# Kernel tuning notes

Hardware: AMD Instinct MI355X
Metric: run time of the kernel (lower is better)

The kernel has to match this reference:

```python
import jax, jax.numpy as jnp
import numpy as np
import math

B, S, D, H, FF = 4, 2048, 1024, 16, 4096
DH = D // H
EPS = 1e-6


def setup_inputs() -> dict:
    key = jax.random.key(0)
    ks = jax.random.split(key, 12)
    s = 0.02
    inp = {
        "x": jax.random.normal(ks[0], (B, S, D), dtype=jnp.float32),
        "mask": jax.random.randint(ks[1], (B, 1, S, S), 0, 2, dtype=jnp.int32),
        # torch Linear y = x @ W.T + b; we store W already transposed as [in, out]
        "Wq": jax.random.normal(ks[2], (D, D), dtype=jnp.float32) * s,
        "bq": jnp.zeros((D,), jnp.float32),
        "Wk": jax.random.normal(ks[3], (D, D), dtype=jnp.float32) * s,
        "bk": jnp.zeros((D,), jnp.float32),
        "Wv": jax.random.normal(ks[4], (D, D), dtype=jnp.float32) * s,
        "bv": jnp.zeros((D,), jnp.float32),
        "Wo": jax.random.normal(ks[5], (D, D), dtype=jnp.float32) * s,
        "bo": jnp.zeros((D,), jnp.float32),
        "ln1_g": jnp.ones((D,), jnp.float32),
        "ln1_b": jnp.zeros((D,), jnp.float32),
        "W1": jax.random.normal(ks[6], (D, FF), dtype=jnp.float32) * s,
        "b1": jnp.zeros((FF,), jnp.float32),
        "W2": jax.random.normal(ks[7], (FF, D), dtype=jnp.float32) * s,
        "b2": jnp.zeros((D,), jnp.float32),
        "ln2_g": jnp.ones((D,), jnp.float32),
        "ln2_b": jnp.zeros((D,), jnp.float32),
    }
    return inp


def _layer_norm(x, g, b):
    m = jnp.mean(x, axis=-1, keepdims=True)
    v = jnp.mean(jnp.square(x - m), axis=-1, keepdims=True)
    return (x - m) * jax.lax.rsqrt(v + EPS) * g + b


def reference(x, mask, Wq, bq, Wk, bk, Wv, bv, Wo, bo,
              ln1_g, ln1_b, W1, b1, W2, b2, ln2_g, ln2_b):
    # ---- multi-head self-attention (dropout = identity, eval mode) ----
    def split_heads(t):  # [B,S,D] -> [B,H,S,DH]
        return t.reshape(B, S, H, DH).transpose(0, 2, 1, 3)

    q = split_heads(x @ Wq + bq)
    k = split_heads(x @ Wk + bk)
    v = split_heads(x @ Wv + bv)

    scores = jnp.einsum("bhqd,bhkd->bhqk", q, k) / math.sqrt(DH)
    scores = jnp.where(mask == 0, jnp.float32(-1e9), scores)
    attn = jax.nn.softmax(scores, axis=-1)
    out = jnp.einsum("bhqk,bhkd->bhqd", attn, v)
    out = out.transpose(0, 2, 1, 3).reshape(B, S, D)
    attn_out = out @ Wo + bo

    # ---- sublayer 1: x + LayerNorm(attn_out)  (post-applied LN, faithful) ----
    x = x + _layer_norm(attn_out, ln1_g, ln1_b)

    # ---- FFN with exact GELU ----
    ff = jax.nn.gelu(x @ W1 + b1, approximate=False) @ W2 + b2

    # ---- sublayer 2 ----
    x = x + _layer_norm(ff, ln2_g, ln2_b)
    return x
```

## Files before the change

kernel.cpp:

```cpp
#include <hip/hip_runtime.h>
#include <hip/hip_bf16.h>

#define BDIM 4
#define SDIM 2048
#define DDIM 1024
#define HDIM 16
#define FFDIM 4096
#define MROWS (BDIM*SDIM)

using bf16 = __hip_bfloat16;
typedef __attribute__((ext_vector_type(8))) short short8;
typedef __attribute__((ext_vector_type(4))) short short4v;
typedef __attribute__((ext_vector_type(4))) float f32x4;

__device__ __forceinline__ f32x4 mfma16(short8 a, short8 b, f32x4 c) {
  return __builtin_amdgcn_mfma_f32_16x16x32_bf16(a, b, c, 0, 0, 0);
}

__device__ __forceinline__ void gll16(const void* g, void* l) {
  __builtin_amdgcn_global_load_lds((const __attribute__((address_space(1))) void*)g,
                                   (__attribute__((address_space(3))) void*)l, 16, 0, 0);
}

template<int EPI>
__global__ __launch_bounds__(256)
void gemm_bt(const bf16* __restrict__ A, const bf16* __restrict__ Bt,
             const float* __restrict__ bias0, const float* __restrict__ bias1,
             const float* __restrict__ bias2,
             void* __restrict__ Cout, int K, int N)
{
  __shared__ bf16 As[128*32];
  __shared__ bf16 Bs[128*32];
  const int tid  = threadIdx.x;
  const int wave = tid >> 6;
  const int lane = tid & 63;
  const int llo  = lane & 15, lhi = lane >> 4;
  const int row0 = blockIdx.y * 128;
  const int col0 = blockIdx.x * 128;
  const int wm = wave >> 1, wn = wave & 1;

  f32x4 acc[4][4];
#pragma unroll
  for (int i = 0; i < 4; i++)
#pragma unroll
    for (int j = 0; j < 4; j++) acc[i][j] = (f32x4){0.f, 0.f, 0.f, 0.f};

  const int c0 = wave * 2, c1 = wave * 2 + 1;
  const size_t arow0 = (size_t)(row0 + c0*16 + (lane >> 2)) * K;
  const size_t arow1 = (size_t)(row0 + c1*16 + (lane >> 2)) * K;
  const size_t brow0 = (size_t)(col0 + c0*16 + (lane >> 2)) * K;
  const size_t brow1 = (size_t)(col0 + c1*16 + (lane >> 2)) * K;
  const int colb = ((lane & 3) ^ ((lane >> 3) & 3)) * 8;

  const int nkt = K >> 5;
  for (int kt = 0; kt < nkt; ++kt) {
    __syncthreads();
    const int kofs = kt * 32 + colb;
    gll16(A  + arow0 + kofs, As + c0*512);
    gll16(A  + arow1 + kofs, As + c1*512);
    gll16(Bt + brow0 + kofs, Bs + c0*512);
    gll16(Bt + brow1 + kofs, Bs + c1*512);
    __syncthreads();
    short8 af[4], bfr[4];
    const int rsw = (lhi ^ ((llo >> 1) & 3)) * 8;
#pragma unroll
    for (int mi = 0; mi < 4; mi++)
      af[mi] = *(const short8*)(As + (wm*64 + mi*16 + llo)*32 + rsw);
#pragma unroll
    for (int ni = 0; ni < 4; ni++)
      bfr[ni] = *(const short8*)(Bs + (wn*64 + ni*16 + llo)*32 + rsw);
#pragma unroll
    for (int mi = 0; mi < 4; mi++)
#pragma unroll
      for (int ni = 0; ni < 4; ni++)
        acc[mi][ni] = mfma16(af[mi], bfr[ni], acc[mi][ni]);
  }

#pragma unroll
  for (int mi = 0; mi < 4; mi++) {
#pragma unroll
    for (int ni = 0; ni < 4; ni++) {
      const int col = col0 + wn*64 + ni*16 + llo;
      float bv;
      if (EPI == 1) {
        const int which = col >> 10, win = col & 1023;
        const float* bp = (which == 0) ? bias0 : ((which == 1) ? bias1 : bias2);
        bv = bp[win];
      } else {
        bv = bias0[col];
      }
      if (EPI == 1) {
        const int which = col >> 10, win = col & 1023;
        const int h = win >> 6, dh = win & 63;
        if (which < 2) {
#pragma unroll
          for (int r = 0; r < 4; r++) {
            const int row = row0 + wm*64 + mi*16 + lhi*4 + r;
            const int b = row >> 11, s = row & 2047;
            float v = acc[mi][ni][r] + bv;
            if (which == 0) v *= 0.125f;
            ((bf16*)Cout)[((((size_t)which*BDIM + b)*HDIM + h)*SDIM + s)*64 + dh] =
                __float2bfloat16(v);
          }
        } else {
          const int row = row0 + wm*64 + mi*16 + lhi*4;
          const int b = row >> 11, s = row & 2047;
          short4v pk;
#pragma unroll
          for (int r = 0; r < 4; r++) {
            bf16 t = __float2bfloat16(acc[mi][ni][r] + bv);
            pk[r] = *(short*)&t;
          }
          bf16* vt = (bf16*)Cout + (size_t)2*BDIM*HDIM*SDIM*64;
          *(short4v*)(vt + (((size_t)b*HDIM + h)*64 + dh)*SDIM + s) = pk;
        }
      } else {
#pragma unroll
        for (int r = 0; r < 4; r++) {
          const int row = row0 + wm*64 + mi*16 + lhi*4 + r;
          float v = acc[mi][ni][r] + bv;
          if (EPI == 0) {
            ((float*)Cout)[(size_t)row * N + col] = v;
          } else {
            float gl = 0.5f * v * (1.f + erff(v * 0.70710678118654752f));
            ((bf16*)Cout)[(size_t)row * N + col] = __float2bfloat16(gl);
          }
        }
      }
    }
  }
}

__global__ __launch_bounds__(512)
void attn_fwd(const bf16* __restrict__ qkv,
              const unsigned long long* __restrict__ mbits,
              bf16* __restrict__ Obuf)
{
  __shared__ bf16 Ks[2][64*64];
  __shared__ bf16 Vs[2][64*64];
  __shared__ bf16 Ps[8][16*64];

  const int tid  = threadIdx.x;
  const int wave = tid >> 6, lane = tid & 63;
  const int llo  = lane & 15, lhi = lane >> 4;
  const int bh = blockIdx.y;
  const int b = bh >> 4, h = bh & 15;
  const int q0 = blockIdx.x * 128;

  const bf16* Qp  = qkv + ((size_t)b*HDIM + h) * (size_t)SDIM * 64;
  const bf16* Kp  = qkv + ((size_t)(BDIM*HDIM) + b*HDIM + h) * (size_t)SDIM * 64;
  const bf16* Vtp = qkv + (size_t)2*BDIM*HDIM*SDIM*64
                        + ((size_t)b*HDIM + h) * (size_t)64 * SDIM;

  short8 qf[2];
  {
    const bf16* qrow = Qp + (size_t)(q0 + wave*16 + llo) * 64;
    qf[0] = *(const short8*)(qrow + lhi*8);
    qf[1] = *(const short8*)(qrow + 32 + lhi*8);
  }

  f32x4 o[4];
#pragma unroll
  for (int n = 0; n < 4; n++) o[n] = (f32x4){0.f, 0.f, 0.f, 0.f};
  float mrun[4], lrun[4];
#pragma unroll
  for (int r = 0; r < 4; r++) { mrun[r] = -INFINITY; lrun[r] = 0.f; }

  const int srow = lane >> 3;
  const int scol = ((lane & 7) ^ srow) * 8;
  const size_t mrow = ((size_t)b*SDIM + q0 + wave*16 + lhi*4) * 32;
  const int sh0 = 31 - llo, sh1 = 15 - llo;

  gll16(Kp + (size_t)(wave*8 + srow)*64 + scol, &Ks[0][wave*512]);
  gll16(Vtp + (size_t)(wave*8 + srow)*SDIM + scol, &Vs[0][wave*512]);
  __syncthreads();

  for (int kt = 0; kt < SDIM/64; ++kt) {
    const int cur = kt & 1;
    if (kt + 1 < SDIM/64) {
      const int k1 = (kt + 1) * 64;
      gll16(Kp + (size_t)(k1 + wave*8 + srow)*64 + scol, &Ks[cur^1][wave*512]);
      gll16(Vtp + (size_t)(wave*8 + srow)*SDIM + k1 + scol, &Vs[cur^1][wave*512]);
    }
    unsigned mlo[4], mhi[4];
#pragma unroll
    for (int r = 0; r < 4; r++) {
      unsigned long long mw = mbits[mrow + (size_t)r*32 + kt];
      mlo[r] = (unsigned)mw; mhi[r] = (unsigned)(mw >> 32);
    }

    float sv[4][4];
    __builtin_amdgcn_s_setprio(1);
#pragma unroll
    for (int n = 0; n < 4; n++) {
      const int krow = (n*16 + llo) * 64;
      const int sw   = llo & 7;
      short8 kf0 = *(const short8*)(&Ks[cur][krow + ((lhi ^ sw) * 8)]);
      short8 kf1 = *(const short8*)(&Ks[cur][krow + (((4 | lhi) ^ sw) * 8)]);
      f32x4 z = (f32x4){0.f, 0.f, 0.f, 0.f};
      z = mfma16(qf[0], kf0, z);
      z = mfma16(qf[1], kf1, z);
#pragma unroll
      for (int r = 0; r < 4; r++) sv[n][r] = z[r];
    }
    __builtin_amdgcn_s_setprio(0);
    float mnew[4], scale[4];
#pragma unroll
    for (int r = 0; r < 4; r++) {
      float rm = fmaxf(fmaxf(sv[0][r], sv[1][r]), fmaxf(sv[2][r], sv[3][r]));
      rm = fmaxf(rm, __shfl_xor(rm, 1));
      rm = fmaxf(rm, __shfl_xor(rm, 2));
      rm = fmaxf(rm, __shfl_xor(rm, 4));
      rm = fmaxf(rm, __shfl_xor(rm, 8));
      mnew[r] = fmaxf(mrun[r], rm);
      scale[r] = __expf(mrun[r] - mnew[r]);
      mrun[r] = mnew[r];
    }
    float rsum[4] = {0.f, 0.f, 0.f, 0.f};
#pragma unroll
    for (int n = 0; n < 4; n++)
#pragma unroll
      for (int r = 0; r < 4; r++) {
        float p = __expf(sv[n][r] - mnew[r]);
        const unsigned w = (n & 2) ? mhi[r] : mlo[r];
        const int sx = ((int)(w << ((n & 1) ? sh1 : sh0))) >> 31;
        p = __uint_as_float(__float_as_uint(p) & (unsigned)sx);
        sv[n][r] = p;
        rsum[r] += p;
      }
#pragma unroll
    for (int r = 0; r < 4; r++) {
      float rs = rsum[r];
      rs += __shfl_xor(rs, 1);
      rs += __shfl_xor(rs, 2);
      rs += __shfl_xor(rs, 4);
      rs += __shfl_xor(rs, 8);
      lrun[r] = lrun[r]*scale[r] + rs;
    }
#pragma unroll
    for (int n = 0; n < 4; n++)
#pragma unroll
      for (int r = 0; r < 4; r++) o[n][r] *= scale[r];
#pragma unroll
    for (int n = 0; n < 4; n++)
#pragma unroll
      for (int r = 0; r < 4; r++) {
        const int prow = lhi*4 + r;
        const int slot = (n*2 + (llo >> 3)) ^ (prow & 7);
        Ps[wave][prow*64 + slot*8 + (llo & 7)] = __float2bfloat16(sv[n][r]);
      }
    __builtin_amdgcn_s_setprio(1);
#pragma unroll
    for (int kk = 0; kk < 2; kk++) {
      const int sl = ((kk*4 + lhi) ^ (llo & 7)) * 8;
      short8 pf = *(const short8*)(&Ps[wave][llo*64 + sl]);
#pragma unroll
      for (int n = 0; n < 4; n++) {
        short8 vf = *(const short8*)(&Vs[cur][(n*16 + llo)*64 + sl]);
        o[n] = mfma16(pf, vf, o[n]);
      }
    }
    __builtin_amdgcn_s_setprio(0);
    __syncthreads();
  }

#pragma unroll
  for (int n = 0; n < 4; n++)
#pragma unroll
    for (int r = 0; r < 4; r++) {
      float v = o[n][r] / lrun[r];
      const int row = q0 + wave*16 + lhi*4 + r;
      const int col = h*64 + n*16 + llo;
      Obuf[((size_t)b*SDIM + row)*DDIM + col] = __float2bfloat16(v);
    }
}

template<bool WB>
__global__ __launch_bounds__(256)
void add_ln(const float* __restrict__ resid, const float* __restrict__ y,
            const float* __restrict__ gam, const float* __restrict__ bet,
            float* __restrict__ outf, bf16* __restrict__ outb)
{
  __shared__ float red[4];
  const int row = blockIdx.x;
  const int t = threadIdx.x;
  float4 v = ((const float4*)(y + (size_t)row*DDIM))[t];
  float s = v.x + v.y + v.z + v.w;
#pragma unroll
  for (int off = 1; off < 64; off <<= 1) s += __shfl_xor(s, off);
  if ((t & 63) == 0) red[t >> 6] = s;
  __syncthreads();
  const float mean = (red[0]+red[1]+red[2]+red[3]) * (1.f/DDIM);
  const float dx = v.x-mean, dy = v.y-mean, dz = v.z-mean, dw = v.w-mean;
  float sq = dx*dx + dy*dy + dz*dz + dw*dw;
#pragma unroll
  for (int off = 1; off < 64; off <<= 1) sq += __shfl_xor(sq, off);
  __syncthreads();
  if ((t & 63) == 0) red[t >> 6] = sq;
  __syncthreads();
  const float var = (red[0]+red[1]+red[2]+red[3]) * (1.f/DDIM);
  const float rst = rsqrtf(var + 1e-6f);
  const float4 g  = ((const float4*)gam)[t];
  const float4 bb = ((const float4*)bet)[t];
  const float4 rv = ((const float4*)(resid + (size_t)row*DDIM))[t];
  float4 ov;
  ov.x = rv.x + dx*rst*g.x + bb.x;
  ov.y = rv.y + dy*rst*g.y + bb.y;
  ov.z = rv.z + dz*rst*g.z + bb.z;
  ov.w = rv.w + dw*rst*g.w + bb.w;
  ((float4*)(outf + (size_t)row*DDIM))[t] = ov;
  if (WB) {
    bf16* ob = outb + (size_t)row*DDIM + t*4;
    ob[0] = __float2bfloat16(ov.x);
    ob[1] = __float2bfloat16(ov.y);
    ob[2] = __float2bfloat16(ov.z);
    ob[3] = __float2bfloat16(ov.w);
  }
}

__global__ __launch_bounds__(256)
void transpose_cast(const float* __restrict__ in, bf16* __restrict__ out,
                    int R, int C)
{
  __shared__ float tile[32][33];
  const int x = threadIdx.x & 31, y = threadIdx.x >> 5;
  const int c0 = blockIdx.x * 32, r0 = blockIdx.y * 32;
#pragma unroll
  for (int i = 0; i < 32; i += 8)
    tile[y + i][x] = in[(size_t)(r0 + y + i)*C + c0 + x];
  __syncthreads();
#pragma unroll
  for (int i = 0; i < 32; i += 8)
    out[(size_t)(c0 + y + i)*R + r0 + x] = __float2bfloat16(tile[x][y + i]);
}

__global__ __launch_bounds__(256)
void cast_to_bf16(const float* __restrict__ in, bf16* __restrict__ out, int n4)
{
  const int i = blockIdx.x * 256 + threadIdx.x;
  if (i < n4) {
    float4 v = ((const float4*)in)[i];
    bf16* o = out + (size_t)i*4;
    o[0] = __float2bfloat16(v.x);
    o[1] = __float2bfloat16(v.y);
    o[2] = __float2bfloat16(v.z);
    o[3] = __float2bfloat16(v.w);
  }
}

__global__ __launch_bounds__(256)
void mask_bits_kernel(const int* __restrict__ mask,
                      unsigned long long* __restrict__ bits)
{
  const int wid = blockIdx.x * 4 + (threadIdx.x >> 6);
  const int lane = threadIdx.x & 63;
  const int m = mask[(size_t)wid * 64 + lane];
  const unsigned long long bal = __ballot(m != 0);
  if (lane == 0) bits[wid] = bal;
}

extern "C" void kernel_launch(void* const* d_in, const int* in_sizes, int n_in,
                              void* d_out, int out_size, void* d_ws, size_t ws_size,
                              hipStream_t stream)
{
  (void)in_sizes; (void)n_in; (void)out_size; (void)ws_size;
  const float* x    = (const float*)d_in[0];
  const int*   mask = (const int*)d_in[1];
  const float* Wq   = (const float*)d_in[2];
  const float* bq   = (const float*)d_in[3];
  const float* Wk   = (const float*)d_in[4];
  const float* bk   = (const float*)d_in[5];
  const float* Wv   = (const float*)d_in[6];
  const float* bv   = (const float*)d_in[7];
  const float* Wo   = (const float*)d_in[8];
  const float* bo   = (const float*)d_in[9];
  const float* ln1g = (const float*)d_in[10];
  const float* ln1b = (const float*)d_in[11];
  const float* W1   = (const float*)d_in[12];
  const float* b1   = (const float*)d_in[13];
  const float* W2   = (const float*)d_in[14];
  const float* b2   = (const float*)d_in[15];
  const float* ln2g = (const float*)d_in[16];
  const float* ln2b = (const float*)d_in[17];
  float* out = (float*)d_out;

  char* ws = (char*)d_ws;
  bf16* xb    = (bf16*)(ws + 0);
  bf16* Wqkvt = (bf16*)(ws + 16777216);
  bf16* Wot   = (bf16*)(ws + 23068672);
  bf16* W1t   = (bf16*)(ws + 25165824);
  bf16* W2t   = (bf16*)(ws + 33554432);
  unsigned long long* mbits = (unsigned long long*)(ws + 41943040);
  bf16* qkv   = (bf16*)(ws + 75497472);
  bf16* obuf  = (bf16*)(ws + 125829120);
  float* aproj = (float*)(ws + 142606336);
  float* x1f   = (float*)(ws + 176160768);
  bf16* x1b = xb;
  bf16* h1  = qkv;
  float* ffb = (float*)(ws + 41943040);

  cast_to_bf16<<<dim3(MROWS*DDIM/4/256), 256, 0, stream>>>(x, xb, MROWS*DDIM/4);
  transpose_cast<<<dim3(32, 32), 256, 0, stream>>>(Wq, Wqkvt, 1024, 1024);
  transpose_cast<<<dim3(32, 32), 256, 0, stream>>>(Wk, Wqkvt + 1024*1024, 1024, 1024);
  transpose_cast<<<dim3(32, 32), 256, 0, stream>>>(Wv, Wqkvt + 2*1024*1024, 1024, 1024);
  transpose_cast<<<dim3(32, 32), 256, 0, stream>>>(Wo, Wot, 1024, 1024);
  transpose_cast<<<dim3(FFDIM/32, 32), 256, 0, stream>>>(W1, W1t, 1024, FFDIM);
  transpose_cast<<<dim3(32, FFDIM/32), 256, 0, stream>>>(W2, W2t, FFDIM, 1024);
  mask_bits_kernel<<<dim3(BDIM*SDIM*SDIM/64/4), 256, 0, stream>>>(mask, mbits);

  gemm_bt<1><<<dim3(3072/128, MROWS/128), 256, 0, stream>>>(
      xb, Wqkvt, bq, bk, bv, qkv, 1024, 3072);
  attn_fwd<<<dim3(SDIM/128, BDIM*HDIM), 512, 0, stream>>>(qkv, mbits, obuf);
  gemm_bt<0><<<dim3(1024/128, MROWS/128), 256, 0, stream>>>(
      obuf, Wot, bo, nullptr, nullptr, aproj, 1024, 1024);
  add_ln<true><<<dim3(MROWS), 256, 0, stream>>>(x, aproj, ln1g, ln1b, x1f, x1b);
  gemm_bt<2><<<dim3(FFDIM/128, MROWS/128), 256, 0, stream>>>(
      x1b, W1t, b1, nullptr, nullptr, h1, 1024, FFDIM);
  gemm_bt<0><<<dim3(1024/128, MROWS/128), 256, 0, stream>>>(
      h1, W2t, b2, nullptr, nullptr, ffb, FFDIM, 1024);
  add_ln<false><<<dim3(MROWS), 256, 0, stream>>>(x1f, ffb, ln2g, ln2b, out, nullptr);
}
```

Baseline: 806.6 us.

## Double-buffer GEMM LDS tiles, use tanh GELU, lazily rescale attention softmax

The GEMM kernel now double-buffers its A/B shared-memory tiles, prefetching the next K slice while the current one feeds MFMAs and cutting one barrier per iteration. The FFN epilogue swaps exact erf GELU for the tanh approximation expressed via exp. The attention softmax skips the max update and output rescale unless the row max grows by more than 8, saving exp and multiply work. The GELU approximation and thresholded rescaling change numerics slightly.

```diff
diff --git a/kernel.cpp b/kernel.cpp
--- a/kernel.cpp
+++ b/kernel.cpp
@@ -29,8 +29,8 @@
              const float* __restrict__ bias2,
              void* __restrict__ Cout, int K, int N)
 {
-  __shared__ bf16 As[128*32];
-  __shared__ bf16 Bs[128*32];
+  __shared__ bf16 As[2][128*32];
+  __shared__ bf16 Bs[2][128*32];
   const int tid  = threadIdx.x;
   const int wave = tid >> 6;
   const int lane = tid & 63;
@@ -53,27 +53,35 @@
   const int colb = ((lane & 3) ^ ((lane >> 3) & 3)) * 8;
 
   const int nkt = K >> 5;
+  gll16(A  + arow0 + colb, As[0] + c0*512);
+  gll16(A  + arow1 + colb, As[0] + c1*512);
+  gll16(Bt + brow0 + colb, Bs[0] + c0*512);
+  gll16(Bt + brow1 + colb, Bs[0] + c1*512);
+  __syncthreads();
+
   for (int kt = 0; kt < nkt; ++kt) {
-    __syncthreads();
-    const int kofs = kt * 32 + colb;
-    gll16(A  + arow0 + kofs, As + c0*512);
-    gll16(A  + arow1 + kofs, As + c1*512);
-    gll16(Bt + brow0 + kofs, Bs + c0*512);
-    gll16(Bt + brow1 + kofs, Bs + c1*512);
-    __syncthreads();
+    const int cur = kt & 1;
+    if (kt + 1 < nkt) {
+      const int kofs = (kt + 1) * 32 + colb;
+      gll16(A  + arow0 + kofs, As[cur^1] + c0*512);
+      gll16(A  + arow1 + kofs, As[cur^1] + c1*512);
+      gll16(Bt + brow0 + kofs, Bs[cur^1] + c0*512);
+      gll16(Bt + brow1 + kofs, Bs[cur^1] + c1*512);
+    }
     short8 af[4], bfr[4];
     const int rsw = (lhi ^ ((llo >> 1) & 3)) * 8;
 #pragma unroll
     for (int mi = 0; mi < 4; mi++)
-      af[mi] = *(const short8*)(As + (wm*64 + mi*16 + llo)*32 + rsw);
+      af[mi] = *(const short8*)(As[cur] + (wm*64 + mi*16 + llo)*32 + rsw);
 #pragma unroll
     for (int ni = 0; ni < 4; ni++)
-      bfr[ni] = *(const short8*)(Bs + (wn*64 + ni*16 + llo)*32 + rsw);
+      bfr[ni] = *(const short8*)(Bs[cur] + (wn*64 + ni*16 + llo)*32 + rsw);
 #pragma unroll
     for (int mi = 0; mi < 4; mi++)
 #pragma unroll
       for (int ni = 0; ni < 4; ni++)
         acc[mi][ni] = mfma16(af[mi], bfr[ni], acc[mi][ni]);
+    __syncthreads();
   }
 
 #pragma unroll
@@ -122,7 +130,8 @@
           if (EPI == 0) {
             ((float*)Cout)[(size_t)row * N + col] = v;
           } else {
-            float gl = 0.5f * v * (1.f + erff(v * 0.70710678118654752f));
+            float u  = 0.79788456080286536f * v * (1.f + 0.044715f * v * v);
+            float gl = v / (1.f + __expf(-2.f * u));
             ((bf16*)Cout)[(size_t)row * N + col] = __float2bfloat16(gl);
           }
         }
@@ -204,7 +213,8 @@
       for (int r = 0; r < 4; r++) sv[n][r] = z[r];
     }
     __builtin_amdgcn_s_setprio(0);
-    float mnew[4], scale[4];
+    float scale[4];
+    bool need = false;
 #pragma unroll
     for (int r = 0; r < 4; r++) {
       float rm = fmaxf(fmaxf(sv[0][r], sv[1][r]), fmaxf(sv[2][r], sv[3][r]));
@@ -212,16 +222,30 @@
       rm = fmaxf(rm, __shfl_xor(rm, 2));
       rm = fmaxf(rm, __shfl_xor(rm, 4));
       rm = fmaxf(rm, __shfl_xor(rm, 8));
-      mnew[r] = fmaxf(mrun[r], rm);
-      scale[r] = __expf(mrun[r] - mnew[r]);
-      mrun[r] = mnew[r];
+      scale[r] = rm;
+      need |= (rm > mrun[r] + 8.f);
+    }
+    if (need) {
+#pragma unroll
+      for (int r = 0; r < 4; r++) {
+        float mnew = fmaxf(mrun[r], scale[r]);
+        scale[r] = __expf(mrun[r] - mnew);
+        mrun[r] = mnew;
+      }
+#pragma unroll
+      for (int n = 0; n < 4; n++)
+#pragma unroll
+        for (int r = 0; r < 4; r++) o[n][r] *= scale[r];
+    } else {
+#pragma unroll
+      for (int r = 0; r < 4; r++) scale[r] = 1.f;
     }
     float rsum[4] = {0.f, 0.f, 0.f, 0.f};
 #pragma unroll
     for (int n = 0; n < 4; n++)
 #pragma unroll
       for (int r = 0; r < 4; r++) {
-        float p = __expf(sv[n][r] - mnew[r]);
+        float p = __expf(sv[n][r] - mrun[r]);
         const unsigned w = (n & 2) ? mhi[r] : mlo[r];
         const int sx = ((int)(w << ((n & 1) ? sh1 : sh0))) >> 31;
         p = __uint_as_float(__float_as_uint(p) & (unsigned)sx);
@@ -237,10 +261,6 @@
       rs += __shfl_xor(rs, 8);
       lrun[r] = lrun[r]*scale[r] + rs;
     }
-#pragma unroll
-    for (int n = 0; n < 4; n++)
-#pragma unroll
-      for (int r = 0; r < 4; r++) o[n][r] *= scale[r];
 #pragma unroll
     for (int n = 0; n < 4; n++)
 #pragma unroll
```

Measured after the change: 834.8 us. 3.5% more time.
